# Kernel tuning notes

Measured on AMD Instinct MI355X. Metric: run time of the kernel, lower is better.

Reference implementation:

```python
import jax, jax.numpy as jnp
import numpy as np

B, S, D, H, V = 4, 1024, 2048, 16, 32000
LAYERS, DFF, HID, NSENT, NLAB = 2, 8192, 100, 3, 3
HD = D // H
LN2 = 0.6931471805599453


def _ln(x, g, b):
    m = jnp.mean(x, axis=-1, keepdims=True)
    v = jnp.mean((x - m) ** 2, axis=-1, keepdims=True)
    return (x - m) * jax.lax.rsqrt(v + 1e-5) * g + b


def setup_inputs():
    key = jax.random.key(0)
    ks = jax.random.split(key, 12)
    s = 0.02
    return dict(
        input_ids=jax.random.randint(ks[0], (B, S), 0, V),
        attention_mask=jnp.ones((B, S), dtype=jnp.int32),
        sentiment=jax.random.normal(ks[1], (B, NSENT), dtype=jnp.float32),
        perplexity=jax.random.uniform(ks[2], (B,), dtype=jnp.float32) + 1.0,
        emb=jax.random.normal(ks[3], (V, D), dtype=jnp.float32) * s,
        ln1_g=jnp.ones((LAYERS, D)), ln1_b=jnp.zeros((LAYERS, D)),
        qkv_w=jax.random.normal(ks[4], (LAYERS, D, 3 * D), dtype=jnp.float32) * s,
        wo_w=jax.random.normal(ks[5], (LAYERS, D, D), dtype=jnp.float32) * s,
        ln2_g=jnp.ones((LAYERS, D)), ln2_b=jnp.zeros((LAYERS, D)),
        w1=jax.random.normal(ks[6], (LAYERS, D, DFF), dtype=jnp.float32) * s,
        w2=jax.random.normal(ks[7], (LAYERS, DFF, D), dtype=jnp.float32) * s,
        lnf_g=jnp.ones((D,)), lnf_b=jnp.zeros((D,)),
        head_w=jax.random.normal(ks[8], (D, V), dtype=jnp.float32) * s,
        red_w=jax.random.normal(ks[9], (D, HID), dtype=jnp.float32) * s,
        red_b=jnp.zeros((HID,)),
        cls_w=jax.random.normal(ks[10], (HID + NSENT + 2, NLAB), dtype=jnp.float32) * s,
        cls_b=jnp.zeros((NLAB,)),
    )


def _lm(input_ids, attention_mask, emb, ln1_g, ln1_b, qkv_w, wo_w, ln2_g, ln2_b, w1, w2, lnf_g, lnf_b, head_w):
    x = emb[input_ids]  # [B,S,D]
    amask = attention_mask.astype(jnp.float32)
    causal = jnp.tril(jnp.ones((S, S), dtype=bool))
    bias = jnp.where(causal[None, None, :, :] & (amask[:, None, None, :] > 0), 0.0, -1e9)
    for l in range(LAYERS):
        h = _ln(x, ln1_g[l], ln1_b[l])
        qkv = h @ qkv_w[l]  # [B,S,3D]
        q, k, v = [t.reshape(B, S, H, HD) for t in jnp.split(qkv, 3, axis=-1)]
        scores = jnp.einsum('bqhd,bkhd->bhqk', q, k) / np.float32(np.sqrt(HD)) + bias
        attn = jax.nn.softmax(scores, axis=-1)
        o = jnp.einsum('bhqk,bkhd->bqhd', attn, v).reshape(B, S, D)
        x = x + o @ wo_w[l]
        h = _ln(x, ln2_g[l], ln2_b[l])
        x = x + jax.nn.gelu(h @ w1[l]) @ w2[l]
    h = _ln(x, lnf_g, lnf_b)
    logits = h @ head_w  # [B,S,V]
    return h, logits


def reference(input_ids, attention_mask, sentiment, perplexity, emb, ln1_g, ln1_b, qkv_w, wo_w, ln2_g, ln2_b, w1, w2, lnf_g, lnf_b, head_w, red_w, red_b, cls_w, cls_b):
    h, logits = _lm(input_ids, attention_mask, emb, ln1_g, ln1_b, qkv_w, wo_w,
                    ln2_g, ln2_b, w1, w2, lnf_g, lnf_b, head_w)
    amask = attention_mask.astype(jnp.float32)
    pooled = jnp.mean(h, axis=1)  # mean over seq -> [B,D]
    # probs = softmax(logits).detach(); gather own token prob; -log2(p)
    lg = jax.lax.stop_gradient(logits)
    logZ = jax.scipy.special.logsumexp(lg, axis=-1)  # [B,S]
    tok_logit = jnp.take_along_axis(lg, input_ids[..., None], axis=-1)[..., 0]
    subword_surp = -(tok_logit - logZ) / LN2 * amask
    mean_surprisal = subword_surp.sum(axis=1) / amask.sum(axis=1)  # [B]
    r = jax.nn.leaky_relu(pooled @ red_w + red_b)  # torch intent: LeakyReLU after reducer
    feats = jnp.concatenate([r, sentiment, perplexity[:, None], mean_surprisal[:, None]], axis=1)
    return feats @ cls_w + cls_b  # [B, NLAB]
```

## Files before the change

kernel.cpp:

```cpp
#include <hip/hip_runtime.h>

typedef unsigned short u16;
typedef __bf16 bf16x8 __attribute__((ext_vector_type(8)));
typedef float f32x4 __attribute__((ext_vector_type(4)));

__device__ __forceinline__ u16 f2bf(float f){
  unsigned u = __float_as_uint(f);
  unsigned r = u + 0x7FFFu + ((u >> 16) & 1u);
  return (u16)(r >> 16);
}
__device__ __forceinline__ float bf2f(u16 v){ return __uint_as_float(((unsigned)v) << 16); }

__device__ __forceinline__ void gload16(const void* g, void* l){
  __builtin_amdgcn_global_load_lds(
      (const __attribute__((address_space(1))) unsigned int*)g,
      (__attribute__((address_space(3))) unsigned int*)l, 16, 0, 0);
}

__global__ __launch_bounds__(256) void transp_k(const float* __restrict__ in, u16* __restrict__ out, int K, int N)
{
  __shared__ float tl[64][65];
  const int n0 = blockIdx.x * 64, k0 = blockIdx.y * 64;
  const int t = threadIdx.x;
  const int r = t >> 4, c4 = t & 15;
#pragma unroll
  for (int i = 0; i < 4; ++i){
    float4 v = *(const float4*)(in + (size_t)(k0 + r + i*16) * N + n0 + c4*4);
    tl[r + i*16][c4*4 + 0] = v.x; tl[r + i*16][c4*4 + 1] = v.y;
    tl[r + i*16][c4*4 + 2] = v.z; tl[r + i*16][c4*4 + 3] = v.w;
  }
  __syncthreads();
#pragma unroll
  for (int i = 0; i < 4; ++i){
    const int n = r + i*16;
    ushort4 o;
    o.x = f2bf(tl[c4*4 + 0][n]); o.y = f2bf(tl[c4*4 + 1][n]);
    o.z = f2bf(tl[c4*4 + 2][n]); o.w = f2bf(tl[c4*4 + 3][n]);
    *(ushort4*)(out + (size_t)(n0 + n) * K + k0 + c4*4) = o;
  }
}

__global__ __launch_bounds__(256) void embed_k(const int* __restrict__ ids, const float* __restrict__ emb, float* __restrict__ x)
{
  const int row = blockIdx.x;
  const int c = blockIdx.y * 256 + threadIdx.x;
  x[(size_t)row * 2048 + c] = emb[(size_t)ids[row] * 2048 + c];
}

__global__ __launch_bounds__(256) void ln_k(const float* __restrict__ x, const float* __restrict__ gw,
                                            const float* __restrict__ bw, u16* __restrict__ o)
{
  const int row = blockIdx.x, t = threadIdx.x;
  const int lane = t & 63, wid = t >> 6;
  const float4* xr = (const float4*)(x + (size_t)row * 2048);
  float4 v1 = xr[t], v2 = xr[t + 256];
  float s1 = v1.x + v1.y + v1.z + v1.w + v2.x + v2.y + v2.z + v2.w;
  float s2 = v1.x*v1.x + v1.y*v1.y + v1.z*v1.z + v1.w*v1.w
           + v2.x*v2.x + v2.y*v2.y + v2.z*v2.z + v2.w*v2.w;
#pragma unroll
  for (int off = 32; off >= 1; off >>= 1){ s1 += __shfl_down(s1, off); s2 += __shfl_down(s2, off); }
  __shared__ float rb[2][4];
  __shared__ float mv[2];
  if (lane == 0){ rb[0][wid] = s1; rb[1][wid] = s2; }
  __syncthreads();
  if (t == 0){
    float a = rb[0][0] + rb[0][1] + rb[0][2] + rb[0][3];
    float q = rb[1][0] + rb[1][1] + rb[1][2] + rb[1][3];
    float mean = a * (1.f/2048.f);
    float var  = q * (1.f/2048.f) - mean*mean;
    mv[0] = mean; mv[1] = rsqrtf(var + 1e-5f);
  }
  __syncthreads();
  const float mean = mv[0], rstd = mv[1];
  const float4* g4 = (const float4*)gw;
  const float4* b4 = (const float4*)bw;
  float4 ga = g4[t], ba = b4[t], gb = g4[t + 256], bb2 = b4[t + 256];
  ushort4 o1, o2;
  o1.x = f2bf((v1.x - mean)*rstd*ga.x + ba.x);
  o1.y = f2bf((v1.y - mean)*rstd*ga.y + ba.y);
  o1.z = f2bf((v1.z - mean)*rstd*ga.z + ba.z);
  o1.w = f2bf((v1.w - mean)*rstd*ga.w + ba.w);
  o2.x = f2bf((v2.x - mean)*rstd*gb.x + bb2.x);
  o2.y = f2bf((v2.y - mean)*rstd*gb.y + bb2.y);
  o2.z = f2bf((v2.z - mean)*rstd*gb.z + bb2.z);
  o2.w = f2bf((v2.w - mean)*rstd*gb.w + bb2.w);
  ((ushort4*)(o + (size_t)row * 2048))[t] = o1;
  ((ushort4*)(o + (size_t)row * 2048))[t + 256] = o2;
}

enum { M_QKV = 0, M_RES = 1, M_GELU = 2, M_LSE = 3 };

template<int MODE, int BM>
__global__ __launch_bounds__(512, 2) void gemm2_k(
    const u16* __restrict__ A, const u16* __restrict__ BT,
    int N, int K, int MB,
    u16* __restrict__ outb, float* __restrict__ outf,
    float* __restrict__ partial, float* __restrict__ tokl,
    const int* __restrict__ ids, u16* __restrict__ vtout)
{
  constexpr int BK  = 32;
  constexpr int ASZ = BM * BK;
  constexpr int BSZ = 256 * BK;
  constexpr int BUF = ASZ + BSZ;
  constexpr int NFR = BM / 32;
  __shared__ u16 lds[3 * BUF];

  const int tid  = threadIdx.x;
  const int wv   = tid >> 6, lane = tid & 63;
  const int wr   = wv >> 2,  wc   = wv & 3;
  const int lg   = lane >> 4, lr  = lane & 15;

  const int nwg = gridDim.x;
  const int bid = blockIdx.x;
  const int swz = ((nwg & 7) == 0) ? ((bid & 7) * (nwg >> 3) + (bid >> 3)) : bid;
  const int bm = swz % MB, bn = swz / MB;
  const int m0 = bm * BM, n0 = bn * 256;

  const int ll = lane >> 3;
  const int cc = lane & 7;
  const int lc = cc ^ ll;
  const int gr = (ll << 1) + (lc >> 2);
  const int gk = (lc & 3) << 3;

  const u16* gA = A  + (size_t)m0 * K + gk;
  const u16* gB = BT + (size_t)n0 * K + gk;

  f32x4 acc[NFR][4];
#pragma unroll
  for (int i = 0; i < NFR; ++i)
#pragma unroll
    for (int j = 0; j < 4; ++j)
#pragma unroll
      for (int r = 0; r < 4; ++r) acc[i][j][r] = 0.f;

  const int nt = K >> 5;

  auto STAGE = [&](int bi, int kt){
    char* bA = (char*)lds + (size_t)bi * BUF * 2;
    char* bB = bA + ASZ * 2;
    const size_t ko = (size_t)kt * 32;
    if constexpr (BM == 256){
      gload16(gA + (size_t)((wv    ) * 16 + gr) * K + ko, bA + (wv    ) * 1024);
      gload16(gA + (size_t)((wv + 8) * 16 + gr) * K + ko, bA + (wv + 8) * 1024);
    } else {
      gload16(gA + (size_t)(wv * 16 + gr) * K + ko, bA + wv * 1024);
    }
    gload16(gB + (size_t)((wv    ) * 16 + gr) * K + ko, bB + (wv    ) * 1024);
    gload16(gB + (size_t)((wv + 8) * 16 + gr) * K + ko, bB + (wv + 8) * 1024);
  };

  STAGE(0, 0);
  STAGE(1, 1);

  for (int t = 0; t < nt; ++t){
    if (t + 1 < nt){
      if constexpr (BM == 256) asm volatile("s_waitcnt vmcnt(4) lgkmcnt(0)" ::: "memory");
      else                     asm volatile("s_waitcnt vmcnt(3) lgkmcnt(0)" ::: "memory");
    } else {
      asm volatile("s_waitcnt vmcnt(0) lgkmcnt(0)" ::: "memory");
    }
    __builtin_amdgcn_s_barrier();
    if (t + 2 < nt) STAGE((t + 2) % 3, t + 2);

    const char* bA = (const char*)lds + (size_t)(t % 3) * BUF * 2;
    const char* bB = bA + ASZ * 2;
    bf16x8 af[NFR], bq[4];
#pragma unroll
    for (int i = 0; i < NFR; ++i){
      const int ra = wr * (BM / 2) + i * 16 + lr;
      const int p = ra >> 1;
      const int slot = (((ra & 1) << 2) | lg) ^ (p & 7);
      af[i] = *(const bf16x8*)(bA + p * 128 + slot * 16);
    }
#pragma unroll
    for (int j = 0; j < 4; ++j){
      const int rb = wc * 64 + j * 16 + lr;
      const int p = rb >> 1;
      const int slot = (((rb & 1) << 2) | lg) ^ (p & 7);
      bq[j] = *(const bf16x8*)(bB + p * 128 + slot * 16);
    }
    __builtin_amdgcn_s_setprio(1);
#pragma unroll
    for (int i = 0; i < NFR; ++i)
#pragma unroll
      for (int j = 0; j < 4; ++j)
        acc[i][j] = __builtin_amdgcn_mfma_f32_16x16x32_bf16(af[i], bq[j], acc[i][j], 0, 0, 0);
    __builtin_amdgcn_s_setprio(0);
  }

#pragma unroll
  for (int i = 0; i < NFR; ++i){
#pragma unroll
    for (int r = 0; r < 4; ++r){
      const int row = m0 + wr * (BM / 2) + i * 16 + lg * 4 + r;
      if constexpr (MODE == M_LSE){
        const int id = ids[row];
        float esum = 0.f;
#pragma unroll
        for (int j = 0; j < 4; ++j){
          const int col = n0 + wc * 64 + j * 16 + lr;
          const float v = acc[i][j][r];
          if (col == id) tokl[row] = v;
          esum += __expf(v);
        }
#pragma unroll
        for (int off = 8; off >= 1; off >>= 1) esum += __shfl_xor(esum, off);
        if (lr == 0) partial[(size_t)row * 500 + bn * 4 + wc] = esum;
      } else {
#pragma unroll
        for (int j = 0; j < 4; ++j){
          const int col = n0 + wc * 64 + j * 16 + lr;
          const float v = acc[i][j][r];
          if constexpr (MODE == M_RES){
            float* pp = outf + (size_t)row * N + col;
            *pp += v;
          } else if constexpr (MODE == M_GELU){
            float u = 0.7978845608028654f * (v + 0.044715f * v * v * v);
            u = fminf(fmaxf(u, -15.f), 15.f);
            const float ex = __expf(2.f * u);
            const float th = (ex - 1.f) / (ex + 1.f);
            outb[(size_t)row * N + col] = f2bf(0.5f * v * (1.f + th));
          } else {
            const u16 uv = f2bf(v);
            if (col < 4096) outb[(size_t)row * 6144 + col] = uv;
            else {
              int dd2 = col - 4096;
              const int hh = dd2 >> 7; dd2 &= 127;
              vtout[(((size_t)((row >> 10) * 16 + hh)) * 128 + dd2) * 1024 + (row & 1023)] = uv;
            }
          }
        }
      }
    }
  }
}

__global__ __launch_bounds__(64) void attn_k(const u16* __restrict__ qkv, const u16* __restrict__ vT, u16* __restrict__ o16)
{
  __shared__ u16 P[16 * 40];
  const int bid = blockIdx.x;
  const int qt = bid & 63, bh = bid >> 6;
  const int h = bh & 15, b = bh >> 4;
  const int lane = threadIdx.x, lg = lane >> 4, lr = lane & 15;
  const int q0 = qt << 4;
  const u16* qrow  = qkv + (size_t)(b * 1024 + q0 + lr) * 6144 + h * 128;
  const u16* krow  = qkv + (size_t)(b * 1024 + lr) * 6144 + 2048 + h * 128;
  const u16* vbase = vT + (size_t)(b * 16 + h) * 128 * 1024;

  bf16x8 qf[4];
#pragma unroll
  for (int c = 0; c < 4; ++c) qf[c] = *(const bf16x8*)(qrow + c * 32 + lg * 8);

  float m[4], l[4];
  f32x4 oacc[8];
#pragma unroll
  for (int r = 0; r < 4; ++r){ m[r] = -1e30f; l[r] = 0.f; }
#pragma unroll
  for (int f = 0; f < 8; ++f)
#pragma unroll
    for (int r = 0; r < 4; ++r) oacc[f][r] = 0.f;

  const float scale = 0.08838834764831845f;
  const int nk2 = (qt >> 1) + 1;
  for (int k2 = 0; k2 < nk2; ++k2){
    float e[2][4];
    float rmax[4];
#pragma unroll
    for (int r = 0; r < 4; ++r) rmax[r] = -1e30f;
#pragma unroll
    for (int hh = 0; hh < 2; ++hh){
      const int kt = k2 * 2 + hh;
      if (kt <= qt){
        f32x4 s;
#pragma unroll
        for (int r = 0; r < 4; ++r) s[r] = 0.f;
#pragma unroll
        for (int c = 0; c < 4; ++c){
          bf16x8 kf = *(const bf16x8*)(krow + (size_t)(kt * 16) * 6144 + c * 32 + lg * 8);
          s = __builtin_amdgcn_mfma_f32_16x16x32_bf16(qf[c], kf, s, 0, 0, 0);
        }
#pragma unroll
        for (int r = 0; r < 4; ++r){
          float sv = s[r] * scale;
          if (kt * 16 + lr > q0 + lg * 4 + r) sv = -1e30f;
          e[hh][r] = sv;
          rmax[r] = fmaxf(rmax[r], sv);
        }
      } else {
#pragma unroll
        for (int r = 0; r < 4; ++r) e[hh][r] = -1e30f;
      }
    }
#pragma unroll
    for (int off = 8; off >= 1; off >>= 1)
#pragma unroll
      for (int r = 0; r < 4; ++r) rmax[r] = fmaxf(rmax[r], __shfl_xor(rmax[r], off));
    float corr[4], rsum[4];
#pragma unroll
    for (int r = 0; r < 4; ++r){
      const float mn = fmaxf(m[r], rmax[r]);
      corr[r] = __expf(m[r] - mn);
      m[r] = mn;
      const float e0 = __expf(e[0][r] - mn);
      const float e1 = __expf(e[1][r] - mn);
      e[0][r] = e0; e[1][r] = e1;
      rsum[r] = e0 + e1;
    }
#pragma unroll
    for (int off = 8; off >= 1; off >>= 1)
#pragma unroll
      for (int r = 0; r < 4; ++r) rsum[r] += __shfl_xor(rsum[r], off);
#pragma unroll
    for (int r = 0; r < 4; ++r) l[r] = l[r] * corr[r] + rsum[r];
#pragma unroll
    for (int hh = 0; hh < 2; ++hh)
#pragma unroll
      for (int r = 0; r < 4; ++r)
        P[(lg * 4 + r) * 40 + hh * 16 + lr] = f2bf(e[hh][r]);
#pragma unroll
    for (int f = 0; f < 8; ++f)
#pragma unroll
      for (int r = 0; r < 4; ++r) oacc[f][r] = oacc[f][r] * corr[r];
    __syncthreads();
    const bf16x8 pa = *(const bf16x8*)((const u16*)P + lr * 40 + lg * 8);
#pragma unroll
    for (int f = 0; f < 8; ++f){
      bf16x8 vb = *(const bf16x8*)(vbase + (size_t)(f * 16 + lr) * 1024 + k2 * 32 + lg * 8);
      oacc[f] = __builtin_amdgcn_mfma_f32_16x16x32_bf16(pa, vb, oacc[f], 0, 0, 0);
    }
    __syncthreads();
  }
  u16* orow = o16 + (size_t)(b * 1024 + q0 + lg * 4) * 2048 + h * 128;
#pragma unroll
  for (int r = 0; r < 4; ++r){
    const float linv = 1.0f / l[r];
#pragma unroll
    for (int f = 0; f < 8; ++f)
      orow[(size_t)r * 2048 + f * 16 + lr] = f2bf(oacc[f][r] * linv);
  }
}

__global__ __launch_bounds__(256) void lse_k(const float* __restrict__ partial, const float* __restrict__ tokl,
                                             const int* __restrict__ amask, float* __restrict__ surp)
{
  const int row = blockIdx.x, t = threadIdx.x, lane = t & 63, wid = t >> 6;
  float s = 0.f;
  if (t < 250) s = partial[(size_t)row * 500 + t] + partial[(size_t)row * 500 + t + 250];
#pragma unroll
  for (int off = 32; off >= 1; off >>= 1) s += __shfl_down(s, off);
  __shared__ float rb[4];
  if (lane == 0) rb[wid] = s;
  __syncthreads();
  if (t == 0){
    const float tot = rb[0] + rb[1] + rb[2] + rb[3];
    surp[row] = (logf(tot) - tokl[row]) * 1.4426950408889634f * (float)amask[row];
  }
}

__global__ __launch_bounds__(256) void pool_k(const u16* __restrict__ h16, float* __restrict__ pooled)
{
  const int d = blockIdx.x * 256 + threadIdx.x;
  const int b = blockIdx.y;
  const u16* p = h16 + (size_t)b * 1024 * 2048 + d;
  float a0 = 0.f, a1 = 0.f, a2 = 0.f, a3 = 0.f;
  for (int s = 0; s < 1024; s += 4){
    a0 += bf2f(p[(size_t)(s + 0) * 2048]);
    a1 += bf2f(p[(size_t)(s + 1) * 2048]);
    a2 += bf2f(p[(size_t)(s + 2) * 2048]);
    a3 += bf2f(p[(size_t)(s + 3) * 2048]);
  }
  pooled[b * 2048 + d] = (a0 + a1 + a2 + a3) * (1.f / 1024.f);
}

__global__ __launch_bounds__(256) void cls_k(const float* __restrict__ pooled, const float* __restrict__ surp,
                                             const int* __restrict__ amask, const float* __restrict__ sent,
                                             const float* __restrict__ ppl, const float* __restrict__ redw,
                                             const float* __restrict__ redb, const float* __restrict__ clsw,
                                             const float* __restrict__ clsb, float* __restrict__ out)
{
  const int b = blockIdx.x, t = threadIdx.x;
  const int lane = t & 63, wid = t >> 6;
  __shared__ float pl[2048];
  __shared__ float feats[112];
  __shared__ float rbuf[2][4];
#pragma unroll
  for (int i = 0; i < 8; ++i) pl[t + i * 256] = pooled[b * 2048 + t + i * 256];
  float ssum = 0.f, msum = 0.f;
#pragma unroll
  for (int i = 0; i < 4; ++i){
    const int s = t + i * 256;
    ssum += surp[b * 1024 + s];
    msum += (float)amask[b * 1024 + s];
  }
#pragma unroll
  for (int off = 32; off >= 1; off >>= 1){ ssum += __shfl_down(ssum, off); msum += __shfl_down(msum, off); }
  if (lane == 0){ rbuf[0][wid] = ssum; rbuf[1][wid] = msum; }
  __syncthreads();
  if (t == 0){
    float a = 0.f, c = 0.f;
    for (int i = 0; i < 4; ++i){ a += rbuf[0][i]; c += rbuf[1][i]; }
    feats[104] = a / c;
  }
  if (t >= 100 && t < 103) feats[t] = sent[b * 3 + (t - 100)];
  if (t == 103) feats[103] = ppl[b];
  if (t < 100){
    float a = redb[t];
    for (int d = 0; d < 2048; ++d) a += pl[d] * redw[d * 100 + t];
    feats[t] = (a > 0.f) ? a : 0.01f * a;
  }
  __syncthreads();
  if (t < 3){
    float a = clsb[t];
    for (int i = 0; i < 105; ++i) a += feats[i] * clsw[i * 3 + t];
    out[b * 3 + t] = a;
  }
}

extern "C" void kernel_launch(void* const* d_in, const int* in_sizes, int n_in,
                              void* d_out, int out_size, void* d_ws, size_t ws_size,
                              hipStream_t stream)
{
  (void)in_sizes; (void)n_in; (void)out_size; (void)ws_size;
  const int*   ids   = (const int*)d_in[0];
  const int*   amask = (const int*)d_in[1];
  const float* sent  = (const float*)d_in[2];
  const float* ppl   = (const float*)d_in[3];
  const float* emb   = (const float*)d_in[4];
  const float* ln1g  = (const float*)d_in[5];
  const float* ln1b  = (const float*)d_in[6];
  const float* qkvw  = (const float*)d_in[7];
  const float* wow   = (const float*)d_in[8];
  const float* ln2g  = (const float*)d_in[9];
  const float* ln2b  = (const float*)d_in[10];
  const float* w1    = (const float*)d_in[11];
  const float* w2    = (const float*)d_in[12];
  const float* lnfg  = (const float*)d_in[13];
  const float* lnfb  = (const float*)d_in[14];
  const float* headw = (const float*)d_in[15];
  const float* redw  = (const float*)d_in[16];
  const float* redb  = (const float*)d_in[17];
  const float* clsw  = (const float*)d_in[18];
  const float* clsb  = (const float*)d_in[19];
  float* out = (float*)d_out;

  char* p = (char*)d_ws;
  u16* wqkvT = (u16*)p; p += (size_t)2 * 6144 * 2048 * 2;
  u16* woT   = (u16*)p; p += (size_t)2 * 2048 * 2048 * 2;
  u16* w1T   = (u16*)p; p += (size_t)2 * 8192 * 2048 * 2;
  u16* w2T   = (u16*)p; p += (size_t)2 * 2048 * 8192 * 2;
  u16* whT   = (u16*)p; p += (size_t)32000 * 2048 * 2;
  float* xbuf = (float*)p; p += (size_t)4096 * 2048 * 4;
  u16* h16   = (u16*)p; p += (size_t)4096 * 2048 * 2;
  u16* qkv16 = (u16*)p;
  u16* vT16  = (u16*)(p + (size_t)4096 * 6144 * 2);
  u16* ffn16 = (u16*)p;
  p += (size_t)4096 * 6144 * 2 + (size_t)4096 * 2048 * 2;
  u16* o16   = (u16*)p; p += (size_t)4096 * 2048 * 2;
  float* partial = (float*)p; p += (size_t)4096 * 500 * 4;
  float* tokl = (float*)p; p += (size_t)4096 * 4;
  float* surp = (float*)p; p += (size_t)4096 * 4;
  float* pooled = (float*)p; p += (size_t)4 * 2048 * 4;

  for (int l = 0; l < 2; ++l){
    transp_k<<<dim3(6144/64, 2048/64), 256, 0, stream>>>(qkvw + (size_t)l*2048*6144, wqkvT + (size_t)l*6144*2048, 2048, 6144);
    transp_k<<<dim3(2048/64, 2048/64), 256, 0, stream>>>(wow  + (size_t)l*2048*2048, woT   + (size_t)l*2048*2048, 2048, 2048);
    transp_k<<<dim3(8192/64, 2048/64), 256, 0, stream>>>(w1   + (size_t)l*2048*8192, w1T   + (size_t)l*8192*2048, 2048, 8192);
    transp_k<<<dim3(2048/64, 8192/64), 256, 0, stream>>>(w2   + (size_t)l*8192*2048, w2T   + (size_t)l*2048*8192, 8192, 2048);
  }
  transp_k<<<dim3(32000/64, 2048/64), 256, 0, stream>>>(headw, whT, 2048, 32000);

  embed_k<<<dim3(4096, 8), 256, 0, stream>>>(ids, emb, xbuf);

  for (int l = 0; l < 2; ++l){
    ln_k<<<4096, 256, 0, stream>>>(xbuf, ln1g + l*2048, ln1b + l*2048, h16);
    gemm2_k<M_QKV,256><<<16*24, 512, 0, stream>>>(h16, wqkvT + (size_t)l*6144*2048, 6144, 2048, 16,
                                                  qkv16, nullptr, nullptr, nullptr, nullptr, vT16);
    attn_k<<<4096, 64, 0, stream>>>(qkv16, vT16, o16);
    gemm2_k<M_RES,128><<<32*8, 512, 0, stream>>>(o16, woT + (size_t)l*2048*2048, 2048, 2048, 32,
                                                 nullptr, xbuf, nullptr, nullptr, nullptr, nullptr);
    ln_k<<<4096, 256, 0, stream>>>(xbuf, ln2g + l*2048, ln2b + l*2048, h16);
    gemm2_k<M_GELU,256><<<16*32, 512, 0, stream>>>(h16, w1T + (size_t)l*8192*2048, 8192, 2048, 16,
                                                   ffn16, nullptr, nullptr, nullptr, nullptr, nullptr);
    gemm2_k<M_RES,128><<<32*8, 512, 0, stream>>>(ffn16, w2T + (size_t)l*2048*8192, 2048, 8192, 32,
                                                 nullptr, xbuf, nullptr, nullptr, nullptr, nullptr);
  }
  ln_k<<<4096, 256, 0, stream>>>(xbuf, lnfg, lnfb, h16);
  gemm2_k<M_LSE,256><<<16*125, 512, 0, stream>>>(h16, whT, 32000, 2048, 16,
                                                 nullptr, nullptr, partial, tokl, ids, nullptr);
  lse_k<<<4096, 256, 0, stream>>>(partial, tokl, amask, surp);
  pool_k<<<dim3(8, 4), 256, 0, stream>>>(h16, pooled);
  cls_k<<<4, 256, 0, stream>>>(pooled, surp, amask, sent, ppl, redw, redb, clsw, clsb, out);
}
```

Baseline: 2.416 ms.

## Switch GEMM to 32x32x16 MFMA tiles with four-slot LDS ring

Replaces the 16x16x32 bf16 MFMA inner loop with 32x32x16 MFMAs. Each wave now holds larger accumulator tiles, and each 32-wide K step is split into two half-K MFMA passes. The larger tiles should cut LDS fragment reads per FLOP and raise MFMA efficiency. The LDS ring grows from 3 to 4 buffers so slot indices can use a bitmask instead of a modulo. The 4-buffer LDS footprint could limit the 2-workgroup occupancy, and the epilogue row/column mapping is rewritten for the 32x32 output layout.

Result: slower. 2.568 ms (+6.3%).

```diff
diff --git a/kernel.cpp b/kernel.cpp
--- a/kernel.cpp
+++ b/kernel.cpp
@@ -3,6 +3,7 @@
 typedef unsigned short u16;
 typedef __bf16 bf16x8 __attribute__((ext_vector_type(8)));
 typedef float f32x4 __attribute__((ext_vector_type(4)));
+typedef float f32x16 __attribute__((ext_vector_type(16)));
 
 __device__ __forceinline__ u16 f2bf(float f){
   unsigned u = __float_as_uint(f);
@@ -91,7 +92,7 @@
 enum { M_QKV = 0, M_RES = 1, M_GELU = 2, M_LSE = 3 };
 
 template<int MODE, int BM>
-__global__ __launch_bounds__(512, 2) void gemm2_k(
+__global__ __launch_bounds__(512, 2) void gemm3_k(
     const u16* __restrict__ A, const u16* __restrict__ BT,
     int N, int K, int MB,
     u16* __restrict__ outb, float* __restrict__ outf,
@@ -102,13 +103,13 @@
   constexpr int ASZ = BM * BK;
   constexpr int BSZ = 256 * BK;
   constexpr int BUF = ASZ + BSZ;
-  constexpr int NFR = BM / 32;
-  __shared__ u16 lds[3 * BUF];
+  constexpr int NFM = BM / 64;
+  __shared__ u16 lds[4 * BUF];
 
   const int tid  = threadIdx.x;
   const int wv   = tid >> 6, lane = tid & 63;
   const int wr   = wv >> 2,  wc   = wv & 3;
-  const int lg   = lane >> 4, lr  = lane & 15;
+  const int l31  = lane & 31, hi = lane >> 5;
 
   const int nwg = gridDim.x;
   const int bid = blockIdx.x;
@@ -125,13 +126,13 @@
   const u16* gA = A  + (size_t)m0 * K + gk;
   const u16* gB = BT + (size_t)n0 * K + gk;
 
-  f32x4 acc[NFR][4];
-#pragma unroll
-  for (int i = 0; i < NFR; ++i)
-#pragma unroll
-    for (int j = 0; j < 4; ++j)
-#pragma unroll
-      for (int r = 0; r < 4; ++r) acc[i][j][r] = 0.f;
+  f32x16 acc[NFM][2];
+#pragma unroll
+  for (int i = 0; i < NFM; ++i)
+#pragma unroll
+    for (int j = 0; j < 2; ++j)
+#pragma unroll
+      for (int r = 0; r < 16; ++r) acc[i][j][r] = 0.f;
 
   const int nt = K >> 5;
 
@@ -152,6 +153,12 @@
   STAGE(0, 0);
   STAGE(1, 1);
 
+  auto FRAG = [&](const char* base, int row, int chunk) -> bf16x8 {
+    const int p = row >> 1;
+    const int slot = (((row & 1) << 2) | chunk) ^ (p & 7);
+    return *(const bf16x8*)(base + p * 128 + slot * 16);
+  };
+
   for (int t = 0; t < nt; ++t){
     if (t + 1 < nt){
       if constexpr (BM == 256) asm volatile("s_waitcnt vmcnt(4) lgkmcnt(0)" ::: "memory");
@@ -160,57 +167,67 @@
       asm volatile("s_waitcnt vmcnt(0) lgkmcnt(0)" ::: "memory");
     }
     __builtin_amdgcn_s_barrier();
-    if (t + 2 < nt) STAGE((t + 2) % 3, t + 2);
-
-    const char* bA = (const char*)lds + (size_t)(t % 3) * BUF * 2;
+    if (t + 2 < nt) STAGE((t + 2) & 3, t + 2);
+
+    const char* bA = (const char*)lds + (size_t)(t & 3) * BUF * 2;
     const char* bB = bA + ASZ * 2;
-    bf16x8 af[NFR], bq[4];
-#pragma unroll
-    for (int i = 0; i < NFR; ++i){
-      const int ra = wr * (BM / 2) + i * 16 + lr;
-      const int p = ra >> 1;
-      const int slot = (((ra & 1) << 2) | lg) ^ (p & 7);
-      af[i] = *(const bf16x8*)(bA + p * 128 + slot * 16);
-    }
-#pragma unroll
-    for (int j = 0; j < 4; ++j){
-      const int rb = wc * 64 + j * 16 + lr;
-      const int p = rb >> 1;
-      const int slot = (((rb & 1) << 2) | lg) ^ (p & 7);
-      bq[j] = *(const bf16x8*)(bB + p * 128 + slot * 16);
-    }
+
+    bf16x8 bq[2][2];
+#pragma unroll
+    for (int j = 0; j < 2; ++j)
+#pragma unroll
+      for (int s = 0; s < 2; ++s)
+        bq[j][s] = FRAG(bB, wc * 64 + j * 32 + l31, s * 2 + hi);
+
+    bf16x8 af0[NFM];
+#pragma unroll
+    for (int i = 0; i < NFM; ++i)
+      af0[i] = FRAG(bA, wr * (BM / 2) + i * 32 + l31, hi);
     __builtin_amdgcn_s_setprio(1);
 #pragma unroll
-    for (int i = 0; i < NFR; ++i)
-#pragma unroll
-      for (int j = 0; j < 4; ++j)
-        acc[i][j] = __builtin_amdgcn_mfma_f32_16x16x32_bf16(af[i], bq[j], acc[i][j], 0, 0, 0);
+    for (int i = 0; i < NFM; ++i)
+#pragma unroll
+      for (int j = 0; j < 2; ++j)
+        acc[i][j] = __builtin_amdgcn_mfma_f32_32x32x16_bf16(af0[i], bq[j][0], acc[i][j], 0, 0, 0);
     __builtin_amdgcn_s_setprio(0);
-  }
-
-#pragma unroll
-  for (int i = 0; i < NFR; ++i){
-#pragma unroll
-    for (int r = 0; r < 4; ++r){
-      const int row = m0 + wr * (BM / 2) + i * 16 + lg * 4 + r;
+
+    bf16x8 af1[NFM];
+#pragma unroll
+    for (int i = 0; i < NFM; ++i)
+      af1[i] = FRAG(bA, wr * (BM / 2) + i * 32 + l31, 2 + hi);
+    __builtin_amdgcn_s_setprio(1);
+#pragma unroll
+    for (int i = 0; i < NFM; ++i)
+#pragma unroll
+      for (int j = 0; j < 2; ++j)
+        acc[i][j] = __builtin_amdgcn_mfma_f32_32x32x16_bf16(af1[i], bq[j][1], acc[i][j], 0, 0, 0);
+    __builtin_amdgcn_s_setprio(0);
+  }
+
+#pragma unroll
+  for (int i = 0; i < NFM; ++i){
+#pragma unroll
+    for (int reg = 0; reg < 16; ++reg){
+      const int rr = (reg & 3) + 8 * (reg >> 2) + 4 * hi;
+      const int row = m0 + wr * (BM / 2) + i * 32 + rr;
       if constexpr (MODE == M_LSE){
         const int id = ids[row];
-        float esum = 0.f;
-#pragma unroll
-        for (int j = 0; j < 4; ++j){
-          const int col = n0 + wc * 64 + j * 16 + lr;
-          const float v = acc[i][j][r];
+        float e = 0.f;
+#pragma unroll
+        for (int j = 0; j < 2; ++j){
+          const int col = n0 + wc * 64 + j * 32 + l31;
+          const float v = acc[i][j][reg];
           if (col == id) tokl[row] = v;
-          esum += __expf(v);
+          e += __expf(v);
         }
 #pragma unroll
-        for (int off = 8; off >= 1; off >>= 1) esum += __shfl_xor(esum, off);
-        if (lr == 0) partial[(size_t)row * 500 + bn * 4 + wc] = esum;
+        for (int off = 16; off >= 1; off >>= 1) e += __shfl_xor(e, off);
+        if (l31 == 0) partial[(size_t)row * 500 + bn * 4 + wc] = e;
       } else {
 #pragma unroll
-        for (int j = 0; j < 4; ++j){
-          const int col = n0 + wc * 64 + j * 16 + lr;
-          const float v = acc[i][j][r];
+        for (int j = 0; j < 2; ++j){
+          const int col = n0 + wc * 64 + j * 32 + l31;
+          const float v = acc[i][j][reg];
           if constexpr (MODE == M_RES){
             float* pp = outf + (size_t)row * N + col;
             *pp += v;
@@ -473,19 +490,19 @@
 
   for (int l = 0; l < 2; ++l){
     ln_k<<<4096, 256, 0, stream>>>(xbuf, ln1g + l*2048, ln1b + l*2048, h16);
-    gemm2_k<M_QKV,256><<<16*24, 512, 0, stream>>>(h16, wqkvT + (size_t)l*6144*2048, 6144, 2048, 16,
+    gemm3_k<M_QKV,256><<<16*24, 512, 0, stream>>>(h16, wqkvT + (size_t)l*6144*2048, 6144, 2048, 16,
                                                   qkv16, nullptr, nullptr, nullptr, nullptr, vT16);
     attn_k<<<4096, 64, 0, stream>>>(qkv16, vT16, o16);
-    gemm2_k<M_RES,128><<<32*8, 512, 0, stream>>>(o16, woT + (size_t)l*2048*2048, 2048, 2048, 32,
+    gemm3_k<M_RES,128><<<32*8, 512, 0, stream>>>(o16, woT + (size_t)l*2048*2048, 2048, 2048, 32,
                                                  nullptr, xbuf, nullptr, nullptr, nullptr, nullptr);
     ln_k<<<4096, 256, 0, stream>>>(xbuf, ln2g + l*2048, ln2b + l*2048, h16);
-    gemm2_k<M_GELU,256><<<16*32, 512, 0, stream>>>(h16, w1T + (size_t)l*8192*2048, 8192, 2048, 16,
+    gemm3_k<M_GELU,256><<<16*32, 512, 0, stream>>>(h16, w1T + (size_t)l*8192*2048, 8192, 2048, 16,
                                                    ffn16, nullptr, nullptr, nullptr, nullptr, nullptr);
-    gemm2_k<M_RES,128><<<32*8, 512, 0, stream>>>(ffn16, w2T + (size_t)l*2048*8192, 2048, 8192, 32,
+    gemm3_k<M_RES,128><<<32*8, 512, 0, stream>>>(ffn16, w2T + (size_t)l*2048*8192, 2048, 8192, 32,
                                                  nullptr, xbuf, nullptr, nullptr, nullptr, nullptr);
   }
   ln_k<<<4096, 256, 0, stream>>>(xbuf, lnfg, lnfb, h16);
-  gemm2_k<M_LSE,256><<<16*125, 512, 0, stream>>>(h16, whT, 32000, 2048, 16,
+  gemm3_k<M_LSE,256><<<16*125, 512, 0, stream>>>(h16, whT, 32000, 2048, 16,
                                                  nullptr, nullptr, partial, tokl, ids, nullptr);
   lse_k<<<4096, 256, 0, stream>>>(partial, tokl, amask, surp);
   pool_k<<<dim3(8, 4), 256, 0, stream>>>(h16, pooled);
```

## Restructure GEMM into 4-stage split-phase pipeline with vectorized V-transpose stores

Applied to the files above, without the earlier changes.

The GEMM kernel moves from a 3-buffer to a 4-buffer LDS ring with prefetch distance 3. Each k-step is split into two halves, and each half issues part of the next tile's global-to-LDS loads between its fragment reads and MFMAs. Barriers and sched_barriers are meant to interleave memory and compute more finely and hide load latency. The QKV epilogue now writes the transposed V output as ushort4 vectors instead of scattered scalar stores, and the QKV GEMM uses BM=128 tiles with twice as many blocks. The extra LDS buffer and extra barriers per iteration may reduce occupancy or add synchronization cost.

Measured after the change: 2.422 ms. No clear change (+0.2%).

```diff
diff --git a/kernel.cpp b/kernel.cpp
--- a/kernel.cpp
+++ b/kernel.cpp
@@ -91,19 +91,19 @@
 enum { M_QKV = 0, M_RES = 1, M_GELU = 2, M_LSE = 3 };
 
 template<int MODE, int BM>
-__global__ __launch_bounds__(512, 2) void gemm2_k(
+__global__ __launch_bounds__(512, 2) void gemm4_k(
     const u16* __restrict__ A, const u16* __restrict__ BT,
     int N, int K, int MB,
     u16* __restrict__ outb, float* __restrict__ outf,
     float* __restrict__ partial, float* __restrict__ tokl,
     const int* __restrict__ ids, u16* __restrict__ vtout)
 {
-  constexpr int BK  = 32;
-  constexpr int ASZ = BM * BK;
-  constexpr int BSZ = 256 * BK;
-  constexpr int BUF = ASZ + BSZ;
-  constexpr int NFR = BM / 32;
-  __shared__ u16 lds[3 * BUF];
+  constexpr int RW   = BM / 2;
+  constexpr int NM   = RW / 16;
+  constexpr int HALF = NM / 2;
+  constexpr int ABYT = BM * 64;
+  constexpr int BUFU = (BM + 256) * 32;
+  __shared__ u16 lds[4 * BUFU];
 
   const int tid  = threadIdx.x;
   const int wv   = tid >> 6, lane = tid & 63;
@@ -125,9 +125,9 @@
   const u16* gA = A  + (size_t)m0 * K + gk;
   const u16* gB = BT + (size_t)n0 * K + gk;
 
-  f32x4 acc[NFR][4];
-#pragma unroll
-  for (int i = 0; i < NFR; ++i)
+  f32x4 acc[NM][4];
+#pragma unroll
+  for (int i = 0; i < NM; ++i)
 #pragma unroll
     for (int j = 0; j < 4; ++j)
 #pragma unroll
@@ -135,65 +135,98 @@
 
   const int nt = K >> 5;
 
-  auto STAGE = [&](int bi, int kt){
-    char* bA = (char*)lds + (size_t)bi * BUF * 2;
-    char* bB = bA + ASZ * 2;
+  auto STAGE_P = [&](int bi, int kt, int part){
+    char* bA = (char*)lds + (size_t)bi * BUFU * 2;
+    char* bB = bA + ABYT;
     const size_t ko = (size_t)kt * 32;
     if constexpr (BM == 256){
-      gload16(gA + (size_t)((wv    ) * 16 + gr) * K + ko, bA + (wv    ) * 1024);
-      gload16(gA + (size_t)((wv + 8) * 16 + gr) * K + ko, bA + (wv + 8) * 1024);
+      if (part == 0){
+        gload16(gA + (size_t)((wv    ) * 16 + gr) * K + ko, bA + (wv    ) * 1024);
+        gload16(gA + (size_t)((wv + 8) * 16 + gr) * K + ko, bA + (wv + 8) * 1024);
+      } else {
+        gload16(gB + (size_t)((wv    ) * 16 + gr) * K + ko, bB + (wv    ) * 1024);
+        gload16(gB + (size_t)((wv + 8) * 16 + gr) * K + ko, bB + (wv + 8) * 1024);
+      }
     } else {
-      gload16(gA + (size_t)(wv * 16 + gr) * K + ko, bA + wv * 1024);
+      if (part == 0){
+        gload16(gA + (size_t)(wv * 16 + gr) * K + ko, bA + wv * 1024);
+        gload16(gB + (size_t)(wv * 16 + gr) * K + ko, bB + wv * 1024);
+      } else {
+        gload16(gB + (size_t)((wv + 8) * 16 + gr) * K + ko, bB + (wv + 8) * 1024);
+      }
     }
-    gload16(gB + (size_t)((wv    ) * 16 + gr) * K + ko, bB + (wv    ) * 1024);
-    gload16(gB + (size_t)((wv + 8) * 16 + gr) * K + ko, bB + (wv + 8) * 1024);
   };
 
-  STAGE(0, 0);
-  STAGE(1, 1);
+  auto FRAG = [&](const char* base, int row) -> bf16x8 {
+    const int p = row >> 1;
+    const int slot = (((row & 1) << 2) | lg) ^ (p & 7);
+    return *(const bf16x8*)(base + p * 128 + slot * 16);
+  };
+
+  STAGE_P(0, 0, 0); STAGE_P(0, 0, 1);
+  STAGE_P(1, 1, 0); STAGE_P(1, 1, 1);
+  STAGE_P(2, 2, 0); STAGE_P(2, 2, 1);
+  if constexpr (BM == 256) asm volatile("s_waitcnt vmcnt(8)" ::: "memory");
+  else                     asm volatile("s_waitcnt vmcnt(6)" ::: "memory");
+  __builtin_amdgcn_s_barrier();
 
   for (int t = 0; t < nt; ++t){
-    if (t + 1 < nt){
-      if constexpr (BM == 256) asm volatile("s_waitcnt vmcnt(4) lgkmcnt(0)" ::: "memory");
-      else                     asm volatile("s_waitcnt vmcnt(3) lgkmcnt(0)" ::: "memory");
-    } else {
-      asm volatile("s_waitcnt vmcnt(0) lgkmcnt(0)" ::: "memory");
-    }
+    const char* bA = (const char*)lds + (size_t)(t & 3) * BUFU * 2;
+    const char* bB = bA + ABYT;
+
+    bf16x8 bq[4];
+#pragma unroll
+    for (int j = 0; j < 4; ++j) bq[j] = FRAG(bB, wc * 64 + j * 16 + lr);
+    bf16x8 af[HALF];
+#pragma unroll
+    for (int i = 0; i < HALF; ++i) af[i] = FRAG(bA, wr * RW + i * 16 + lr);
+    if (t + 3 < nt) STAGE_P((t + 3) & 3, t + 3, 0);
     __builtin_amdgcn_s_barrier();
-    if (t + 2 < nt) STAGE((t + 2) % 3, t + 2);
-
-    const char* bA = (const char*)lds + (size_t)(t % 3) * BUF * 2;
-    const char* bB = bA + ASZ * 2;
-    bf16x8 af[NFR], bq[4];
-#pragma unroll
-    for (int i = 0; i < NFR; ++i){
-      const int ra = wr * (BM / 2) + i * 16 + lr;
-      const int p = ra >> 1;
-      const int slot = (((ra & 1) << 2) | lg) ^ (p & 7);
-      af[i] = *(const bf16x8*)(bA + p * 128 + slot * 16);
-    }
-#pragma unroll
-    for (int j = 0; j < 4; ++j){
-      const int rb = wc * 64 + j * 16 + lr;
-      const int p = rb >> 1;
-      const int slot = (((rb & 1) << 2) | lg) ^ (p & 7);
-      bq[j] = *(const bf16x8*)(bB + p * 128 + slot * 16);
-    }
+    asm volatile("s_waitcnt lgkmcnt(0)" ::: "memory");
+    __builtin_amdgcn_sched_barrier(0);
     __builtin_amdgcn_s_setprio(1);
 #pragma unroll
-    for (int i = 0; i < NFR; ++i)
+    for (int i = 0; i < HALF; ++i)
 #pragma unroll
       for (int j = 0; j < 4; ++j)
         acc[i][j] = __builtin_amdgcn_mfma_f32_16x16x32_bf16(af[i], bq[j], acc[i][j], 0, 0, 0);
     __builtin_amdgcn_s_setprio(0);
-  }
-
-#pragma unroll
-  for (int i = 0; i < NFR; ++i){
-#pragma unroll
-    for (int r = 0; r < 4; ++r){
-      const int row = m0 + wr * (BM / 2) + i * 16 + lg * 4 + r;
-      if constexpr (MODE == M_LSE){
+    __builtin_amdgcn_s_barrier();
+
+    bf16x8 ag[HALF];
+#pragma unroll
+    for (int i = 0; i < HALF; ++i) ag[i] = FRAG(bA, wr * RW + (HALF + i) * 16 + lr);
+    if (t + 3 < nt) STAGE_P((t + 3) & 3, t + 3, 1);
+    __builtin_amdgcn_s_barrier();
+    asm volatile("s_waitcnt lgkmcnt(0)" ::: "memory");
+    __builtin_amdgcn_sched_barrier(0);
+    __builtin_amdgcn_s_setprio(1);
+#pragma unroll
+    for (int i = 0; i < HALF; ++i)
+#pragma unroll
+      for (int j = 0; j < 4; ++j)
+        acc[HALF + i][j] = __builtin_amdgcn_mfma_f32_16x16x32_bf16(ag[i], bq[j], acc[HALF + i][j], 0, 0, 0);
+    __builtin_amdgcn_s_setprio(0);
+    if (t + 1 < nt){
+      if (t + 3 < nt){
+        if constexpr (BM == 256) asm volatile("s_waitcnt vmcnt(8)" ::: "memory");
+        else                     asm volatile("s_waitcnt vmcnt(6)" ::: "memory");
+      } else if (t + 2 < nt){
+        if constexpr (BM == 256) asm volatile("s_waitcnt vmcnt(4)" ::: "memory");
+        else                     asm volatile("s_waitcnt vmcnt(3)" ::: "memory");
+      } else {
+        asm volatile("s_waitcnt vmcnt(0)" ::: "memory");
+      }
+      __builtin_amdgcn_s_barrier();
+    }
+  }
+
+#pragma unroll
+  for (int i = 0; i < NM; ++i){
+    if constexpr (MODE == M_LSE){
+#pragma unroll
+      for (int r = 0; r < 4; ++r){
+        const int row = m0 + wr * RW + i * 16 + lg * 4 + r;
         const int id = ids[row];
         float esum = 0.f;
 #pragma unroll
@@ -206,7 +239,32 @@
 #pragma unroll
         for (int off = 8; off >= 1; off >>= 1) esum += __shfl_xor(esum, off);
         if (lr == 0) partial[(size_t)row * 500 + bn * 4 + wc] = esum;
-      } else {
+      }
+    } else if constexpr (MODE == M_QKV){
+#pragma unroll
+      for (int j = 0; j < 4; ++j){
+        const int colb = n0 + wc * 64 + j * 16;
+        if (colb < 4096){
+#pragma unroll
+          for (int r = 0; r < 4; ++r){
+            const int row = m0 + wr * RW + i * 16 + lg * 4 + r;
+            outb[(size_t)row * 6144 + colb + lr] = f2bf(acc[i][j][r]);
+          }
+        } else {
+          const int srow = m0 + wr * RW + i * 16 + lg * 4;
+          const int b = srow >> 10, s = srow & 1023;
+          int dd = colb + lr - 4096;
+          const int hh = dd >> 7; dd &= 127;
+          ushort4 o;
+          o.x = f2bf(acc[i][j][0]); o.y = f2bf(acc[i][j][1]);
+          o.z = f2bf(acc[i][j][2]); o.w = f2bf(acc[i][j][3]);
+          *(ushort4*)(vtout + ((size_t)(b * 16 + hh) * 128 + dd) * 1024 + s) = o;
+        }
+      }
+    } else {
+#pragma unroll
+      for (int r = 0; r < 4; ++r){
+        const int row = m0 + wr * RW + i * 16 + lg * 4 + r;
 #pragma unroll
         for (int j = 0; j < 4; ++j){
           const int col = n0 + wc * 64 + j * 16 + lr;
@@ -214,20 +272,12 @@
           if constexpr (MODE == M_RES){
             float* pp = outf + (size_t)row * N + col;
             *pp += v;
-          } else if constexpr (MODE == M_GELU){
+          } else {
             float u = 0.7978845608028654f * (v + 0.044715f * v * v * v);
             u = fminf(fmaxf(u, -15.f), 15.f);
             const float ex = __expf(2.f * u);
             const float th = (ex - 1.f) / (ex + 1.f);
             outb[(size_t)row * N + col] = f2bf(0.5f * v * (1.f + th));
-          } else {
-            const u16 uv = f2bf(v);
-            if (col < 4096) outb[(size_t)row * 6144 + col] = uv;
-            else {
-              int dd2 = col - 4096;
-              const int hh = dd2 >> 7; dd2 &= 127;
-              vtout[(((size_t)((row >> 10) * 16 + hh)) * 128 + dd2) * 1024 + (row & 1023)] = uv;
-            }
           }
         }
       }
@@ -473,19 +523,19 @@
 
   for (int l = 0; l < 2; ++l){
     ln_k<<<4096, 256, 0, stream>>>(xbuf, ln1g + l*2048, ln1b + l*2048, h16);
-    gemm2_k<M_QKV,256><<<16*24, 512, 0, stream>>>(h16, wqkvT + (size_t)l*6144*2048, 6144, 2048, 16,
+    gemm4_k<M_QKV,128><<<32*24, 512, 0, stream>>>(h16, wqkvT + (size_t)l*6144*2048, 6144, 2048, 32,
                                                   qkv16, nullptr, nullptr, nullptr, nullptr, vT16);
     attn_k<<<4096, 64, 0, stream>>>(qkv16, vT16, o16);
-    gemm2_k<M_RES,128><<<32*8, 512, 0, stream>>>(o16, woT + (size_t)l*2048*2048, 2048, 2048, 32,
+    gemm4_k<M_RES,128><<<32*8, 512, 0, stream>>>(o16, woT + (size_t)l*2048*2048, 2048, 2048, 32,
                                                  nullptr, xbuf, nullptr, nullptr, nullptr, nullptr);
     ln_k<<<4096, 256, 0, stream>>>(xbuf, ln2g + l*2048, ln2b + l*2048, h16);
-    gemm2_k<M_GELU,256><<<16*32, 512, 0, stream>>>(h16, w1T + (size_t)l*8192*2048, 8192, 2048, 16,
+    gemm4_k<M_GELU,256><<<16*32, 512, 0, stream>>>(h16, w1T + (size_t)l*8192*2048, 8192, 2048, 16,
                                                    ffn16, nullptr, nullptr, nullptr, nullptr, nullptr);
-    gemm2_k<M_RES,128><<<32*8, 512, 0, stream>>>(ffn16, w2T + (size_t)l*2048*8192, 2048, 8192, 32,
+    gemm4_k<M_RES,128><<<32*8, 512, 0, stream>>>(ffn16, w2T + (size_t)l*2048*8192, 2048, 8192, 32,
                                                  nullptr, xbuf, nullptr, nullptr, nullptr, nullptr);
   }
   ln_k<<<4096, 256, 0, stream>>>(xbuf, lnfg, lnfb, h16);
-  gemm2_k<M_LSE,256><<<16*125, 512, 0, stream>>>(h16, whT, 32000, 2048, 16,
+  gemm4_k<M_LSE,256><<<16*125, 512, 0, stream>>>(h16, whT, 32000, 2048, 16,
                                                  nullptr, nullptr, partial, tokl, ids, nullptr);
   lse_k<<<4096, 256, 0, stream>>>(partial, tokl, amask, surp);
   pool_k<<<dim3(8, 4), 256, 0, stream>>>(h16, pooled);
```

## Load B fragments directly from global into registers, stage only A in LDS

Applied to the files above, without the earlier changes.

The GEMM kernel no longer stages the weight (B) tile through LDS. Each wave loads its own B fragments straight from global memory into registers one K-step ahead, using double-buffered register sets, while A keeps a 4-deep LDS ring. This cuts LDS footprint and LDS read traffic, and the QKV epilogue writes V-transpose as packed 4-element stores. QKV also moves to a BM=128 tile with a larger grid. The cost is redundant global B reads across the wave rows (they now bypass LDS sharing), plus higher register pressure.

After: 3.035 ms. 1.26x slower.

```diff
diff --git a/kernel.cpp b/kernel.cpp
--- a/kernel.cpp
+++ b/kernel.cpp
@@ -91,19 +91,16 @@
 enum { M_QKV = 0, M_RES = 1, M_GELU = 2, M_LSE = 3 };
 
 template<int MODE, int BM>
-__global__ __launch_bounds__(512, 2) void gemm2_k(
+__global__ __launch_bounds__(512, 2) void gemm5_k(
     const u16* __restrict__ A, const u16* __restrict__ BT,
     int N, int K, int MB,
     u16* __restrict__ outb, float* __restrict__ outf,
     float* __restrict__ partial, float* __restrict__ tokl,
     const int* __restrict__ ids, u16* __restrict__ vtout)
 {
-  constexpr int BK  = 32;
-  constexpr int ASZ = BM * BK;
-  constexpr int BSZ = 256 * BK;
-  constexpr int BUF = ASZ + BSZ;
   constexpr int NFR = BM / 32;
-  __shared__ u16 lds[3 * BUF];
+  constexpr int ATU = BM * 32;
+  __shared__ u16 lds[4 * ATU];
 
   const int tid  = threadIdx.x;
   const int wv   = tid >> 6, lane = tid & 63;
@@ -122,8 +119,8 @@
   const int gr = (ll << 1) + (lc >> 2);
   const int gk = (lc & 3) << 3;
 
-  const u16* gA = A  + (size_t)m0 * K + gk;
-  const u16* gB = BT + (size_t)n0 * K + gk;
+  const u16* gA  = A  + (size_t)m0 * K + gk;
+  const u16* gBr = BT + (size_t)(n0 + wc * 64 + lr) * K + lg * 8;
 
   f32x4 acc[NFR][4];
 #pragma unroll
@@ -136,8 +133,7 @@
   const int nt = K >> 5;
 
   auto STAGE = [&](int bi, int kt){
-    char* bA = (char*)lds + (size_t)bi * BUF * 2;
-    char* bB = bA + ASZ * 2;
+    char* bA = (char*)lds + (size_t)bi * ATU * 2;
     const size_t ko = (size_t)kt * 32;
     if constexpr (BM == 256){
       gload16(gA + (size_t)((wv    ) * 16 + gr) * K + ko, bA + (wv    ) * 1024);
@@ -145,55 +141,61 @@
     } else {
       gload16(gA + (size_t)(wv * 16 + gr) * K + ko, bA + wv * 1024);
     }
-    gload16(gB + (size_t)((wv    ) * 16 + gr) * K + ko, bB + (wv    ) * 1024);
-    gload16(gB + (size_t)((wv + 8) * 16 + gr) * K + ko, bB + (wv + 8) * 1024);
   };
 
+  auto FRAG = [&](const char* base, int row) -> bf16x8 {
+    const int p = row >> 1;
+    const int slot = (((row & 1) << 2) | lg) ^ (p & 7);
+    return *(const bf16x8*)(base + p * 128 + slot * 16);
+  };
+
+  auto PHASE = [&](int t, bf16x8 (&bc)[4], bf16x8 (&bn)[4]){
+    if (t + 1 < nt){
+#pragma unroll
+      for (int j = 0; j < 4; ++j)
+        bn[j] = *(const bf16x8*)(gBr + (size_t)j * 16 * K + (t + 1) * 32);
+    }
+    if (t + 2 < nt) STAGE((t + 2) & 3, t + 2);
+    if (t + 2 < nt){
+      if constexpr (BM == 256) asm volatile("s_waitcnt vmcnt(6)" ::: "memory");
+      else                     asm volatile("s_waitcnt vmcnt(5)" ::: "memory");
+    } else if (t + 1 < nt){
+      asm volatile("s_waitcnt vmcnt(4)" ::: "memory");
+    } else {
+      asm volatile("s_waitcnt vmcnt(0)" ::: "memory");
+    }
+    __builtin_amdgcn_s_barrier();
+    const char* bA = (const char*)lds + (size_t)(t & 3) * ATU * 2;
+    bf16x8 af[NFR];
+#pragma unroll
+    for (int i = 0; i < NFR; ++i) af[i] = FRAG(bA, wr * (BM / 2) + i * 16 + lr);
+    __builtin_amdgcn_s_setprio(1);
+#pragma unroll
+    for (int i = 0; i < NFR; ++i)
+#pragma unroll
+      for (int j = 0; j < 4; ++j)
+        acc[i][j] = __builtin_amdgcn_mfma_f32_16x16x32_bf16(af[i], bc[j], acc[i][j], 0, 0, 0);
+    __builtin_amdgcn_s_setprio(0);
+  };
+
+  bf16x8 b0[4], b1[4];
+#pragma unroll
+  for (int j = 0; j < 4; ++j)
+    b0[j] = *(const bf16x8*)(gBr + (size_t)j * 16 * K);
   STAGE(0, 0);
   STAGE(1, 1);
 
-  for (int t = 0; t < nt; ++t){
-    if (t + 1 < nt){
-      if constexpr (BM == 256) asm volatile("s_waitcnt vmcnt(4) lgkmcnt(0)" ::: "memory");
-      else                     asm volatile("s_waitcnt vmcnt(3) lgkmcnt(0)" ::: "memory");
-    } else {
-      asm volatile("s_waitcnt vmcnt(0) lgkmcnt(0)" ::: "memory");
-    }
-    __builtin_amdgcn_s_barrier();
-    if (t + 2 < nt) STAGE((t + 2) % 3, t + 2);
-
-    const char* bA = (const char*)lds + (size_t)(t % 3) * BUF * 2;
-    const char* bB = bA + ASZ * 2;
-    bf16x8 af[NFR], bq[4];
-#pragma unroll
-    for (int i = 0; i < NFR; ++i){
-      const int ra = wr * (BM / 2) + i * 16 + lr;
-      const int p = ra >> 1;
-      const int slot = (((ra & 1) << 2) | lg) ^ (p & 7);
-      af[i] = *(const bf16x8*)(bA + p * 128 + slot * 16);
-    }
-#pragma unroll
-    for (int j = 0; j < 4; ++j){
-      const int rb = wc * 64 + j * 16 + lr;
-      const int p = rb >> 1;
-      const int slot = (((rb & 1) << 2) | lg) ^ (p & 7);
-      bq[j] = *(const bf16x8*)(bB + p * 128 + slot * 16);
-    }
-    __builtin_amdgcn_s_setprio(1);
-#pragma unroll
-    for (int i = 0; i < NFR; ++i)
-#pragma unroll
-      for (int j = 0; j < 4; ++j)
-        acc[i][j] = __builtin_amdgcn_mfma_f32_16x16x32_bf16(af[i], bq[j], acc[i][j], 0, 0, 0);
-    __builtin_amdgcn_s_setprio(0);
+  for (int t = 0; t < nt; t += 2){
+    PHASE(t,     b0, b1);
+    PHASE(t + 1, b1, b0);
   }
 
 #pragma unroll
   for (int i = 0; i < NFR; ++i){
-#pragma unroll
-    for (int r = 0; r < 4; ++r){
-      const int row = m0 + wr * (BM / 2) + i * 16 + lg * 4 + r;
-      if constexpr (MODE == M_LSE){
+    if constexpr (MODE == M_LSE){
+#pragma unroll
+      for (int r = 0; r < 4; ++r){
+        const int row = m0 + wr * (BM / 2) + i * 16 + lg * 4 + r;
         const int id = ids[row];
         float esum = 0.f;
 #pragma unroll
@@ -206,7 +208,32 @@
 #pragma unroll
         for (int off = 8; off >= 1; off >>= 1) esum += __shfl_xor(esum, off);
         if (lr == 0) partial[(size_t)row * 500 + bn * 4 + wc] = esum;
-      } else {
+      }
+    } else if constexpr (MODE == M_QKV){
+#pragma unroll
+      for (int j = 0; j < 4; ++j){
+        const int colb = n0 + wc * 64 + j * 16;
+        if (colb < 4096){
+#pragma unroll
+          for (int r = 0; r < 4; ++r){
+            const int row = m0 + wr * (BM / 2) + i * 16 + lg * 4 + r;
+            outb[(size_t)row * 6144 + colb + lr] = f2bf(acc[i][j][r]);
+          }
+        } else {
+          const int srow = m0 + wr * (BM / 2) + i * 16 + lg * 4;
+          const int b = srow >> 10, s = srow & 1023;
+          int dd = colb + lr - 4096;
+          const int hh = dd >> 7; dd &= 127;
+          ushort4 o;
+          o.x = f2bf(acc[i][j][0]); o.y = f2bf(acc[i][j][1]);
+          o.z = f2bf(acc[i][j][2]); o.w = f2bf(acc[i][j][3]);
+          *(ushort4*)(vtout + ((size_t)(b * 16 + hh) * 128 + dd) * 1024 + s) = o;
+        }
+      }
+    } else {
+#pragma unroll
+      for (int r = 0; r < 4; ++r){
+        const int row = m0 + wr * (BM / 2) + i * 16 + lg * 4 + r;
 #pragma unroll
         for (int j = 0; j < 4; ++j){
           const int col = n0 + wc * 64 + j * 16 + lr;
@@ -214,20 +241,12 @@
           if constexpr (MODE == M_RES){
             float* pp = outf + (size_t)row * N + col;
             *pp += v;
-          } else if constexpr (MODE == M_GELU){
+          } else {
             float u = 0.7978845608028654f * (v + 0.044715f * v * v * v);
             u = fminf(fmaxf(u, -15.f), 15.f);
             const float ex = __expf(2.f * u);
             const float th = (ex - 1.f) / (ex + 1.f);
             outb[(size_t)row * N + col] = f2bf(0.5f * v * (1.f + th));
-          } else {
-            const u16 uv = f2bf(v);
-            if (col < 4096) outb[(size_t)row * 6144 + col] = uv;
-            else {
-              int dd2 = col - 4096;
-              const int hh = dd2 >> 7; dd2 &= 127;
-              vtout[(((size_t)((row >> 10) * 16 + hh)) * 128 + dd2) * 1024 + (row & 1023)] = uv;
-            }
           }
         }
       }
@@ -473,19 +492,19 @@
 
   for (int l = 0; l < 2; ++l){
     ln_k<<<4096, 256, 0, stream>>>(xbuf, ln1g + l*2048, ln1b + l*2048, h16);
-    gemm2_k<M_QKV,256><<<16*24, 512, 0, stream>>>(h16, wqkvT + (size_t)l*6144*2048, 6144, 2048, 16,
+    gemm5_k<M_QKV,128><<<32*24, 512, 0, stream>>>(h16, wqkvT + (size_t)l*6144*2048, 6144, 2048, 32,
                                                   qkv16, nullptr, nullptr, nullptr, nullptr, vT16);
     attn_k<<<4096, 64, 0, stream>>>(qkv16, vT16, o16);
-    gemm2_k<M_RES,128><<<32*8, 512, 0, stream>>>(o16, woT + (size_t)l*2048*2048, 2048, 2048, 32,
+    gemm5_k<M_RES,128><<<32*8, 512, 0, stream>>>(o16, woT + (size_t)l*2048*2048, 2048, 2048, 32,
                                                  nullptr, xbuf, nullptr, nullptr, nullptr, nullptr);
     ln_k<<<4096, 256, 0, stream>>>(xbuf, ln2g + l*2048, ln2b + l*2048, h16);
-    gemm2_k<M_GELU,256><<<16*32, 512, 0, stream>>>(h16, w1T + (size_t)l*8192*2048, 8192, 2048, 16,
+    gemm5_k<M_GELU,256><<<16*32, 512, 0, stream>>>(h16, w1T + (size_t)l*8192*2048, 8192, 2048, 16,
                                                    ffn16, nullptr, nullptr, nullptr, nullptr, nullptr);
-    gemm2_k<M_RES,128><<<32*8, 512, 0, stream>>>(ffn16, w2T + (size_t)l*2048*8192, 2048, 8192, 32,
+    gemm5_k<M_RES,128><<<32*8, 512, 0, stream>>>(ffn16, w2T + (size_t)l*2048*8192, 2048, 8192, 32,
                                                  nullptr, xbuf, nullptr, nullptr, nullptr, nullptr);
   }
   ln_k<<<4096, 256, 0, stream>>>(xbuf, lnfg, lnfb, h16);
-  gemm2_k<M_LSE,256><<<16*125, 512, 0, stream>>>(h16, whT, 32000, 2048, 16,
+  gemm5_k<M_LSE,256><<<16*125, 512, 0, stream>>>(h16, whT, 32000, 2048, 16,
                                                  nullptr, nullptr, partial, tokl, ids, nullptr);
   lse_k<<<4096, 256, 0, stream>>>(partial, tokl, amask, surp);
   pool_k<<<dim3(8, 4), 256, 0, stream>>>(h16, pooled);
```
